# Performance work log

Measured on AMD Instinct MI355X. Metric: run time of the kernel, lower is better.

Reference implementation:

```python
import jax, jax.numpy as jnp
import numpy as np

B, N, K = 32, 65536, 2  # batch, nodes, residual dim per node


def setup_inputs() -> dict:
    key = jax.random.key(0)
    k0, k1, k2, k3, k4 = jax.random.split(key, 5)
    r = jax.random.normal(k0, (B, N, K), dtype=jnp.float32)
    w = jax.random.uniform(k1, (B, N, 2), dtype=jnp.float32)  # [conf, node_lambda]
    J_p = jax.random.normal(k2, (B, N, K, 6), dtype=jnp.float32)
    J_d = jax.random.normal(k3, (B, N, K, 1), dtype=jnp.float32)
    lmbda = jax.random.uniform(k4, (1, 1, 1), dtype=jnp.float32)
    return {"r": r, "w": w, "J_p": J_p, "J_d": J_d, "lmbda": lmbda}


def reference(r, w, J_p, J_d, lmbda):
    conf = w[..., 0:1][..., None]          # (B,N,1,1)
    node_lambda = w[..., 1:2]              # (B,N,1)

    cJp = conf * J_p                       # (B,N,K,6)
    cJd = conf * J_d                       # (B,N,K,1)

    H_pp = jnp.einsum('bnki,bnkj->bij', J_p, cJp)              # (B,6,6)
    H_pd = jnp.einsum('bnki,bnkj->bnij', J_p, cJd)             # (B,N,6,1)
    H_dd = jnp.einsum('bnk,bnk->bn', J_d[..., 0], cJd[..., 0])[..., None]  # (B,N,1)

    cr = conf[..., 0] * r                  # (B,N,K)
    g_p = jnp.einsum('bnki,bnk->bi', J_p, cr)[..., None]       # (B,6,1)
    g_d = jnp.einsum('bnk,bnk->bn', J_d[..., 0], cr)[..., None]  # (B,N,1)

    eye6 = jnp.eye(6, dtype=r.dtype)[None]                     # (1,6,6)
    H_pp = H_pp + lmbda * eye6
    H_dd = H_dd + lmbda + node_lambda                          # (B,N,1)

    inv_H_dd = 1.0 / (H_dd + 1e-6)                             # (B,N,1)
    H_pd_inv = H_pd * inv_H_dd[..., None]                      # (B,N,6,1)

    # Schur complement: H_eff = H_pp - sum_n H_pd * inv(H_dd) * H_pd^T
    H_eff = H_pp - jnp.einsum('bnik,bnjk->bij', H_pd_inv, H_pd)  # (B,6,6)
    H_eff = 0.5 * (H_eff + jnp.swapaxes(H_eff, -1, -2))
    H_eff = H_eff + 1e-3 * eye6

    g_eff = g_p - jnp.sum(H_pd_inv * g_d[..., None], axis=1)   # (B,6,1)

    delta_pose = jnp.linalg.solve(H_eff, g_eff)                # (B,6,1)

    # back-substitution for depth updates
    v = jnp.einsum('bnik,bi->bnk', H_pd, delta_pose[..., 0])   # (B,N,1)
    delta_depth = inv_H_dd * (g_d - v)                          # (B,N,1)

    return delta_pose[..., 0], delta_depth
```

## Files before the change

### kernel.cpp

```cpp
#include <hip/hip_runtime.h>

#define BN_B 32
#define BN_N 65536
#define BLOCKS_PER_B 64
#define THREADS 256

__device__ __forceinline__ void point_core(
    const float* __restrict__ r, const float* __restrict__ w,
    const float* __restrict__ J_p, const float* __restrict__ J_d,
    size_t p, float lam,
    float jpa[6], float jpb[6], float& c, float& cr0, float& cr1,
    float hpd[6], float& gd, float& ihdd)
{
    float2 wv = *(const float2*)(w + p * 2);
    float2 rv = *(const float2*)(r + p * 2);
    float2 jd = *(const float2*)(J_d + p * 2);
    float4 jp0 = *(const float4*)(J_p + p * 12);
    float4 jp1 = *(const float4*)(J_p + p * 12 + 4);
    float4 jp2 = *(const float4*)(J_p + p * 12 + 8);
    c = wv.x;
    float nl = wv.y;
    jpa[0] = jp0.x; jpa[1] = jp0.y; jpa[2] = jp0.z; jpa[3] = jp0.w; jpa[4] = jp1.x; jpa[5] = jp1.y;
    jpb[0] = jp1.z; jpb[1] = jp1.w; jpb[2] = jp2.x; jpb[3] = jp2.y; jpb[4] = jp2.z; jpb[5] = jp2.w;
    float cjd0 = c * jd.x, cjd1 = c * jd.y;
#pragma unroll
    for (int i = 0; i < 6; ++i) hpd[i] = jpa[i] * cjd0 + jpb[i] * cjd1;
    float hdd = jd.x * cjd0 + jd.y * cjd1;
    cr0 = c * rv.x; cr1 = c * rv.y;
    gd = jd.x * cr0 + jd.y * cr1;
    ihdd = 1.0f / (hdd + lam + nl + 1e-6f);
}

__global__ __launch_bounds__(THREADS) void k_reduce(
    const float* __restrict__ r, const float* __restrict__ w,
    const float* __restrict__ J_p, const float* __restrict__ J_d,
    const float* __restrict__ lmbda, float* __restrict__ partials)
{
    const int b = blockIdx.y;
    const int blk = blockIdx.x;
    const float lam = lmbda[0];

    float acc[27];
#pragma unroll
    for (int i = 0; i < 27; ++i) acc[i] = 0.0f;

    const int n0 = blk * (BN_N / BLOCKS_PER_B);
    const int n1 = n0 + (BN_N / BLOCKS_PER_B);
    const size_t baseP = (size_t)b * BN_N;

    for (int n = n0 + (int)threadIdx.x; n < n1; n += THREADS) {
        size_t p = baseP + n;
        float jpa[6], jpb[6], hpd[6];
        float c, cr0, cr1, gd, ihdd;
        point_core(r, w, J_p, J_d, p, lam, jpa, jpb, c, cr0, cr1, hpd, gd, ihdd);

        int t = 0;
#pragma unroll
        for (int i = 0; i < 6; ++i) {
            float ca = c * jpa[i];
            float cb = c * jpb[i];
            float hs = ihdd * hpd[i];
#pragma unroll
            for (int j = i; j < 6; ++j, ++t)
                acc[t] += ca * jpa[j] + cb * jpb[j] - hs * hpd[j];
            acc[21 + i] += jpa[i] * cr0 + jpb[i] * cr1 - hs * gd;
        }
    }

#pragma unroll
    for (int i = 0; i < 27; ++i) {
        float v = acc[i];
#pragma unroll
        for (int off = 32; off > 0; off >>= 1) v += __shfl_down(v, off);
        acc[i] = v;
    }

    __shared__ float red[4][27];
    const int wave = threadIdx.x >> 6;
    const int lane = threadIdx.x & 63;
    if (lane == 0) {
#pragma unroll
        for (int i = 0; i < 27; ++i) red[wave][i] = acc[i];
    }
    __syncthreads();
    if (threadIdx.x < 27) {
        float s = red[0][threadIdx.x] + red[1][threadIdx.x] +
                  red[2][threadIdx.x] + red[3][threadIdx.x];
        partials[((size_t)b * BLOCKS_PER_B + blk) * 27 + threadIdx.x] = s;
    }
}

__global__ void k_solve(const float* __restrict__ partials,
                        const float* __restrict__ lmbda,
                        float* __restrict__ out)
{
    const int b = blockIdx.x;
    __shared__ float sum27[27];
    if (threadIdx.x < 27) {
        float s = 0.0f;
        for (int p = 0; p < BLOCKS_PER_B; ++p)
            s += partials[((size_t)b * BLOCKS_PER_B + p) * 27 + threadIdx.x];
        sum27[threadIdx.x] = s;
    }
    __syncthreads();
    if (threadIdx.x == 0) {
        const float lam = lmbda[0];
        float A[6][7];
        int t = 0;
        for (int i = 0; i < 6; ++i)
            for (int j = i; j < 6; ++j, ++t) { A[i][j] = sum27[t]; A[j][i] = sum27[t]; }
        for (int i = 0; i < 6; ++i) A[i][i] += lam + 0.001f;
        for (int i = 0; i < 6; ++i) A[i][6] = sum27[21 + i];

        for (int col = 0; col < 6; ++col) {
            int piv = col;
            float best = fabsf(A[col][col]);
            for (int rw = col + 1; rw < 6; ++rw) {
                float v = fabsf(A[rw][col]);
                if (v > best) { best = v; piv = rw; }
            }
            if (piv != col) {
                for (int j = 0; j < 7; ++j) {
                    float tmp = A[col][j]; A[col][j] = A[piv][j]; A[piv][j] = tmp;
                }
            }
            float inv = 1.0f / A[col][col];
            for (int rw = col + 1; rw < 6; ++rw) {
                float f = A[rw][col] * inv;
                for (int j = col; j < 7; ++j) A[rw][j] -= f * A[col][j];
            }
        }
        float x[6];
        for (int i = 5; i >= 0; --i) {
            float s = A[i][6];
            for (int j = i + 1; j < 6; ++j) s -= A[i][j] * x[j];
            x[i] = s / A[i][i];
        }
        for (int i = 0; i < 6; ++i) out[b * 6 + i] = x[i];
    }
}

__global__ __launch_bounds__(THREADS) void k_depth(
    const float* __restrict__ r, const float* __restrict__ w,
    const float* __restrict__ J_p, const float* __restrict__ J_d,
    const float* __restrict__ lmbda, const float* __restrict__ dp,
    float* __restrict__ out_depth)
{
    const int b = blockIdx.y;
    const int blk = blockIdx.x;
    const float lam = lmbda[0];
    float d0 = dp[b * 6 + 0], d1 = dp[b * 6 + 1], d2 = dp[b * 6 + 2];
    float d3 = dp[b * 6 + 3], d4 = dp[b * 6 + 4], d5 = dp[b * 6 + 5];

    const int n0 = blk * (BN_N / BLOCKS_PER_B);
    const int n1 = n0 + (BN_N / BLOCKS_PER_B);
    const size_t baseP = (size_t)b * BN_N;

    for (int n = n0 + (int)threadIdx.x; n < n1; n += THREADS) {
        size_t p = baseP + n;
        float jpa[6], jpb[6], hpd[6];
        float c, cr0, cr1, gd, ihdd;
        point_core(r, w, J_p, J_d, p, lam, jpa, jpb, c, cr0, cr1, hpd, gd, ihdd);
        float v = hpd[0] * d0 + hpd[1] * d1 + hpd[2] * d2 +
                  hpd[3] * d3 + hpd[4] * d4 + hpd[5] * d5;
        out_depth[p] = ihdd * (gd - v);
    }
}

extern "C" void kernel_launch(void* const* d_in, const int* in_sizes, int n_in,
                              void* d_out, int out_size, void* d_ws, size_t ws_size,
                              hipStream_t stream) {
    const float* r     = (const float*)d_in[0];
    const float* w     = (const float*)d_in[1];
    const float* J_p   = (const float*)d_in[2];
    const float* J_d   = (const float*)d_in[3];
    const float* lmbda = (const float*)d_in[4];
    float* out = (float*)d_out;
    float* partials = (float*)d_ws;

    dim3 grid(BLOCKS_PER_B, BN_B);
    k_reduce<<<grid, THREADS, 0, stream>>>(r, w, J_p, J_d, lmbda, partials);
    k_solve<<<dim3(BN_B), 32, 0, stream>>>(partials, lmbda, out);
    k_depth<<<grid, THREADS, 0, stream>>>(r, w, J_p, J_d, lmbda, out, out + 192);
}
```

Measured before the change: 62.52 us.

## Cache compact fp16 per-point state in reduce pass for cheaper depth back-substitution

The reduce kernel now also writes a 16-byte fp16 record per point: the six H_pd*inv(H_dd) terms and inv(H_dd)*g_d. The depth kernel reads only that record instead of reloading and recomputing from the full 72-byte inputs. This lowers total HBM traffic across the two memory-bound passes, at the cost of a 32 MB workspace write. Storing the terms in half precision risks larger error in the depth output. The new path is used only when the workspace is large enough; otherwise the original kernels run.

```diff
diff --git a/kernel.cpp b/kernel.cpp
--- a/kernel.cpp
+++ b/kernel.cpp
@@ -4,6 +4,14 @@
 #define BN_N 65536
 #define BLOCKS_PER_B 64
 #define THREADS 256
+
+typedef _Float16 half_t;
+struct alignas(16) Half8 { half_t h[8]; };
+union StateU { Half8 s; uint4 u; };
+
+#define STATE_OFFSET (256 * 1024)
+#define STATE_BYTES ((size_t)BN_B * BN_N * 16)
+#define WS_NEEDED (STATE_OFFSET + STATE_BYTES)
 
 __device__ __forceinline__ void point_core(
     const float* __restrict__ r, const float* __restrict__ w,
@@ -31,10 +39,12 @@
     ihdd = 1.0f / (hdd + lam + nl + 1e-6f);
 }
 
+template <bool WRITE_STATE>
 __global__ __launch_bounds__(THREADS) void k_reduce(
     const float* __restrict__ r, const float* __restrict__ w,
     const float* __restrict__ J_p, const float* __restrict__ J_d,
-    const float* __restrict__ lmbda, float* __restrict__ partials)
+    const float* __restrict__ lmbda, float* __restrict__ partials,
+    uint4* __restrict__ state)
 {
     const int b = blockIdx.y;
     const int blk = blockIdx.x;
@@ -54,6 +64,7 @@
         float c, cr0, cr1, gd, ihdd;
         point_core(r, w, J_p, J_d, p, lam, jpa, jpb, c, cr0, cr1, hpd, gd, ihdd);
 
+        StateU su;
         int t = 0;
 #pragma unroll
         for (int i = 0; i < 6; ++i) {
@@ -64,6 +75,12 @@
             for (int j = i; j < 6; ++j, ++t)
                 acc[t] += ca * jpa[j] + cb * jpb[j] - hs * hpd[j];
             acc[21 + i] += jpa[i] * cr0 + jpb[i] * cr1 - hs * gd;
+            if (WRITE_STATE) su.s.h[i] = (half_t)hs;
+        }
+        if (WRITE_STATE) {
+            su.s.h[6] = (half_t)(ihdd * gd);
+            su.s.h[7] = (half_t)0.0f;
+            state[p] = su.u;
         }
     }
 
@@ -140,6 +157,31 @@
     }
 }
 
+__global__ __launch_bounds__(THREADS) void k_depth2(
+    const uint4* __restrict__ state, const float* __restrict__ dp,
+    float* __restrict__ out_depth)
+{
+    const int b = blockIdx.y;
+    const int blk = blockIdx.x;
+    float d[6];
+#pragma unroll
+    for (int i = 0; i < 6; ++i) d[i] = dp[b * 6 + i];
+
+    const int n0 = blk * (BN_N / BLOCKS_PER_B);
+    const int n1 = n0 + (BN_N / BLOCKS_PER_B);
+    const size_t baseP = (size_t)b * BN_N;
+
+    for (int n = n0 + (int)threadIdx.x; n < n1; n += THREADS) {
+        size_t p = baseP + n;
+        StateU su;
+        su.u = state[p];
+        float v = 0.0f;
+#pragma unroll
+        for (int i = 0; i < 6; ++i) v += (float)su.s.h[i] * d[i];
+        out_depth[p] = (float)su.s.h[6] - v;
+    }
+}
+
 __global__ __launch_bounds__(THREADS) void k_depth(
     const float* __restrict__ r, const float* __restrict__ w,
     const float* __restrict__ J_p, const float* __restrict__ J_d,
@@ -177,9 +219,16 @@
     const float* lmbda = (const float*)d_in[4];
     float* out = (float*)d_out;
     float* partials = (float*)d_ws;
+    uint4* state = (uint4*)((char*)d_ws + STATE_OFFSET);
 
     dim3 grid(BLOCKS_PER_B, BN_B);
-    k_reduce<<<grid, THREADS, 0, stream>>>(r, w, J_p, J_d, lmbda, partials);
-    k_solve<<<dim3(BN_B), 32, 0, stream>>>(partials, lmbda, out);
-    k_depth<<<grid, THREADS, 0, stream>>>(r, w, J_p, J_d, lmbda, out, out + 192);
-}
+    if (ws_size >= WS_NEEDED) {
+        k_reduce<true><<<grid, THREADS, 0, stream>>>(r, w, J_p, J_d, lmbda, partials, state);
+        k_solve<<<dim3(BN_B), 32, 0, stream>>>(partials, lmbda, out);
+        k_depth2<<<grid, THREADS, 0, stream>>>(state, out, out + 192);
+    } else {
+        k_reduce<false><<<grid, THREADS, 0, stream>>>(r, w, J_p, J_d, lmbda, partials, nullptr);
+        k_solve<<<dim3(BN_B), 32, 0, stream>>>(partials, lmbda, out);
+        k_depth<<<grid, THREADS, 0, stream>>>(r, w, J_p, J_d, lmbda, out, out + 192);
+    }
+}
```

Measured after the change: 51.59 us. 17.5% less time.
